# Kernel tuning notes

Measured on AMD Instinct MI355X. Metric: run time of the kernel, lower is better.

## Reference

```python
import jax, jax.numpy as jnp
import numpy as np

B, L, H_IN, N_FLOWS = 65536, 256, 300, 4


def householder(v, z):
    # z_new = z - 2 * v * (v . z) / ||v||^2   (fused; same math as vvT bmm chain)
    vz = jnp.sum(v * z, axis=1, keepdims=True)      # [B,1]
    norm_sq = jnp.sum(v * v, axis=1, keepdims=True)  # [B,1]
    return z - 2.0 * v * (vz / norm_sq)


def setup_inputs() -> dict:
    key = jax.random.key(0)
    ks = jax.random.split(key, 6)
    z = jax.random.normal(ks[0], (B, L), dtype=jnp.float32)
    h = jax.random.normal(ks[1], (B, H_IN), dtype=jnp.float32)
    W0 = jax.random.normal(ks[2], (L, H_IN), dtype=jnp.float32) * 0.05
    b0 = jax.random.normal(ks[3], (L,), dtype=jnp.float32) * 0.05
    Ws = jax.random.normal(ks[4], (N_FLOWS - 1, L, L), dtype=jnp.float32) * 0.05
    bs = jax.random.normal(ks[5], (N_FLOWS - 1, L), dtype=jnp.float32) * 0.05
    return {"z": z, "h": h, "W0": W0, "b0": b0, "Ws": Ws, "bs": bs}


def reference(z, h, W0, b0, Ws, bs):
    v = h @ W0.T + b0            # Linear(300 -> L)
    z = householder(v, z)
    for i in range(Ws.shape[0]):  # small fixed chain (n_flows-1)
        v = v @ Ws[i].T + bs[i]   # Linear(L -> L)
        z = householder(v, z)
    return z
```

## Files before the change

kernel.cpp:

```cpp
#include <hip/hip_runtime.h>

typedef __attribute__((ext_vector_type(4))) float f32x4;
typedef __attribute__((ext_vector_type(8))) short bf16x8;
typedef __attribute__((ext_vector_type(2))) unsigned int u32x2;
typedef __attribute__((ext_vector_type(4))) unsigned int u32x4;
typedef unsigned short ushort_t;

#define B_ROWS 65536
#define L_DIM  256
#define H_IN_D 300
#define H_PAD  320
#define BM     64
#define LDW    328
#define NTH    256

__device__ __forceinline__ ushort_t f2bf(float f) {
  unsigned u = __builtin_bit_cast(unsigned, f);
  unsigned r = u + 0x7fffu + ((u >> 16) & 1u);
  return (ushort_t)(r >> 16);
}
__device__ __forceinline__ unsigned pk2(float lo, float hi) {
  return (unsigned)f2bf(lo) | ((unsigned)f2bf(hi) << 16);
}
__device__ __forceinline__ float bflo(unsigned u) { return __builtin_bit_cast(float, u << 16); }
__device__ __forceinline__ float bfhi(unsigned u) { return __builtin_bit_cast(float, u & 0xffff0000u); }

__global__ void cvt_w(const float* __restrict__ W0, const float* __restrict__ Ws,
                      ushort_t* __restrict__ W0b, ushort_t* __restrict__ Wsb) {
  int i = blockIdx.x * blockDim.x + threadIdx.x;
  int stride = gridDim.x * blockDim.x;
  for (int t = i; t < 256 * H_PAD; t += stride) {
    int n = t / H_PAD, k = t - n * H_PAD;
    W0b[t] = (k < H_IN_D) ? f2bf(W0[n * H_IN_D + k]) : (ushort_t)0;
  }
  for (int t = i; t < 3 * 256 * 256; t += stride) Wsb[t] = f2bf(Ws[t]);
}

template<int KSTEPS>
__device__ __forceinline__ void gemm_acc(
    const ushort_t* __restrict__ Slds,
    const ushort_t* __restrict__ Wg, int ldb,
    int wave, int r, int g, f32x4 (&acc)[4][4])
{
  const ushort_t* xb = Wg + (wave * 64 + r) * ldb + g * 8;
  const ushort_t* yb = Slds + r * LDW + g * 8;
#pragma unroll
  for (int ks = 0; ks < KSTEPS; ++ks) {
    bf16x8 x[4];
#pragma unroll
    for (int nt = 0; nt < 4; ++nt) x[nt] = *(const bf16x8*)(xb + nt * 16 * ldb + ks * 32);
    bf16x8 y[4];
#pragma unroll
    for (int mt = 0; mt < 4; ++mt) y[mt] = *(const bf16x8*)(yb + mt * 16 * LDW + ks * 32);
#pragma unroll
    for (int nt = 0; nt < 4; ++nt) {
      acc[nt][0] = __builtin_amdgcn_mfma_f32_16x16x32_bf16(x[nt], y[0], acc[nt][0], 0, 0, 0);
      acc[nt][1] = __builtin_amdgcn_mfma_f32_16x16x32_bf16(x[nt], y[1], acc[nt][1], 0, 0, 0);
      acc[nt][2] = __builtin_amdgcn_mfma_f32_16x16x32_bf16(x[nt], y[2], acc[nt][2], 0, 0, 0);
      acc[nt][3] = __builtin_amdgcn_mfma_f32_16x16x32_bf16(x[nt], y[3], acc[nt][3], 0, 0, 0);
    }
  }
}

__device__ __forceinline__ void epi_write(
    f32x4 (&acc)[4][4], const float* __restrict__ bias,
    ushort_t* __restrict__ Slds, int wave, int r, int g)
{
#pragma unroll
  for (int nt = 0; nt < 4; ++nt) {
    const int n0 = wave * 64 + nt * 16 + g * 4;
    f32x4 bv = *(const f32x4*)(bias + n0);
#pragma unroll
    for (int mt = 0; mt < 4; ++mt) {
      float v0 = acc[nt][mt][0] + bv[0];
      float v1 = acc[nt][mt][1] + bv[1];
      float v2 = acc[nt][mt][2] + bv[2];
      float v3 = acc[nt][mt][3] + bv[3];
      u32x2 p; p[0] = pk2(v0, v1); p[1] = pk2(v2, v3);
      *(u32x2*)&Slds[(mt * 16 + r) * LDW + n0] = p;
    }
  }
}

__device__ __forceinline__ void dot_update(const ushort_t* __restrict__ V,
                                           int wave, int r, int g, float (&zr)[64])
{
  const ushort_t* vp = V + (wave * 16 + r) * LDW + g * 64;
  float vz = 0.f, vv = 0.f;
#pragma unroll
  for (int jb = 0; jb < 8; ++jb) {
    u32x4 q = *(const u32x4*)(vp + jb * 8);
#pragma unroll
    for (int w = 0; w < 4; ++w) {
      unsigned u = q[w];
      float f0 = bflo(u), f1 = bfhi(u);
      int i = jb * 8 + w * 2;
      vz = fmaf(f0, zr[i], vz);     vv = fmaf(f0, f0, vv);
      vz = fmaf(f1, zr[i + 1], vz); vv = fmaf(f1, f1, vv);
    }
  }
  vz += __shfl_xor(vz, 16); vv += __shfl_xor(vv, 16);
  vz += __shfl_xor(vz, 32); vv += __shfl_xor(vv, 32);
  float a = 2.f * vz / vv;
#pragma unroll
  for (int jb = 0; jb < 8; ++jb) {
    u32x4 q = *(const u32x4*)(vp + jb * 8);
#pragma unroll
    for (int w = 0; w < 4; ++w) {
      unsigned u = q[w];
      int i = jb * 8 + w * 2;
      zr[i]     = fmaf(-a, bflo(u), zr[i]);
      zr[i + 1] = fmaf(-a, bfhi(u), zr[i + 1]);
    }
  }
}

__global__ __launch_bounds__(NTH, 2) void flow_fused(
    const float* __restrict__ z, const float* __restrict__ h,
    const ushort_t* __restrict__ W0b, const float* __restrict__ b0,
    const ushort_t* __restrict__ Wsb, const float* __restrict__ bs,
    float* __restrict__ out)
{
  __shared__ __align__(16) ushort_t S[BM * LDW];

  const int tid  = threadIdx.x;
  const int wave = tid >> 6;
  const int lane = tid & 63;
  const int r    = lane & 15;
  const int g    = lane >> 4;
  const int row0 = blockIdx.x * BM;

  for (int row = wave; row < BM; row += 4) {
    const float* hrow = h + (row0 + row) * H_IN_D;
    f32x4 m4 = *(const f32x4*)(hrow + 4 * lane);
    u32x2 pm; pm[0] = pk2(m4[0], m4[1]); pm[1] = pk2(m4[2], m4[3]);
    *(u32x2*)&S[row * LDW + 4 * lane] = pm;
    if (lane < 16) {
      f32x4 t4 = {0.f, 0.f, 0.f, 0.f};
      if (lane < 11) t4 = *(const f32x4*)(hrow + 256 + 4 * lane);
      u32x2 pt; pt[0] = pk2(t4[0], t4[1]); pt[1] = pk2(t4[2], t4[3]);
      *(u32x2*)&S[row * LDW + 256 + 4 * lane] = pt;
    }
  }

  float zr[64];
  const int zrow = wave * 16 + r;
  {
    const float* zp = z + (row0 + zrow) * L_DIM + g * 64;
#pragma unroll
    for (int j = 0; j < 16; ++j) {
      f32x4 v = *(const f32x4*)(zp + j * 4);
      zr[j * 4 + 0] = v[0]; zr[j * 4 + 1] = v[1];
      zr[j * 4 + 2] = v[2]; zr[j * 4 + 3] = v[3];
    }
  }

  __syncthreads();

  {
    f32x4 acc[4][4];
#pragma unroll
    for (int a = 0; a < 4; ++a)
#pragma unroll
      for (int b = 0; b < 4; ++b) { acc[a][b][0]=0.f; acc[a][b][1]=0.f; acc[a][b][2]=0.f; acc[a][b][3]=0.f; }
    gemm_acc<10>(S, W0b, H_PAD, wave, r, g, acc);
    __syncthreads();
    epi_write(acc, b0, S, wave, r, g);
  }
  __syncthreads();
  dot_update(S, wave, r, g, zr);

#pragma unroll
  for (int s = 0; s < 3; ++s) {
    f32x4 acc[4][4];
#pragma unroll
    for (int a = 0; a < 4; ++a)
#pragma unroll
      for (int b = 0; b < 4; ++b) { acc[a][b][0]=0.f; acc[a][b][1]=0.f; acc[a][b][2]=0.f; acc[a][b][3]=0.f; }
    gemm_acc<8>(S, Wsb + s * 256 * 256, 256, wave, r, g, acc);
    __syncthreads();
    epi_write(acc, bs + s * 256, S, wave, r, g);
    __syncthreads();
    dot_update(S, wave, r, g, zr);
  }

  {
    float* op = out + (row0 + zrow) * L_DIM + g * 64;
#pragma unroll
    for (int j = 0; j < 16; ++j) {
      f32x4 v;
      v[0] = zr[j * 4 + 0]; v[1] = zr[j * 4 + 1];
      v[2] = zr[j * 4 + 2]; v[3] = zr[j * 4 + 3];
      *(f32x4*)(op + j * 4) = v;
    }
  }
}

extern "C" void kernel_launch(void* const* d_in, const int* in_sizes, int n_in,
                              void* d_out, int out_size, void* d_ws, size_t ws_size,
                              hipStream_t stream) {
  const float* z  = (const float*)d_in[0];
  const float* h  = (const float*)d_in[1];
  const float* W0 = (const float*)d_in[2];
  const float* b0 = (const float*)d_in[3];
  const float* Ws = (const float*)d_in[4];
  const float* bs = (const float*)d_in[5];
  float* out = (float*)d_out;

  ushort_t* W0b = (ushort_t*)d_ws;
  ushort_t* Wsb = W0b + 256 * H_PAD;

  hipLaunchKernelGGL(cvt_w, dim3(256), dim3(NTH), 0, stream, W0, Ws, W0b, Wsb);
  hipLaunchKernelGGL(flow_fused, dim3(B_ROWS / BM), dim3(NTH), 0, stream,
                     z, h, W0b, b0, Wsb, bs, out);
}
```

Baseline: 134.7 us.

## Precompose linear chain into per-stage matrices applied directly to h

Because each v is an affine function of h, the weights are composed on device (M_i = W_i·M_{i-1}, c_i = W_i c_{i-1} + b_i) by small prep kernels, and the main kernel computes every v from h with independent K=320 GEMMs. This removes the serial dependence on bf16-rounded v and drops the LDS write-back of v between stages. The Householder dot products are now done on the MFMA accumulators in registers, with a cross-wave reduction through shared memory. In exchange the per-row GEMM work rises (K=320 instead of 256 for three stages), three extra serial prep launches are added, and composing the products may change rounding behavior.

```diff
diff --git a/kernel.cpp b/kernel.cpp
--- a/kernel.cpp
+++ b/kernel.cpp
@@ -3,15 +3,13 @@
 typedef __attribute__((ext_vector_type(4))) float f32x4;
 typedef __attribute__((ext_vector_type(8))) short bf16x8;
 typedef __attribute__((ext_vector_type(2))) unsigned int u32x2;
-typedef __attribute__((ext_vector_type(4))) unsigned int u32x4;
 typedef unsigned short ushort_t;
 
-#define B_ROWS 65536
 #define L_DIM  256
 #define H_IN_D 300
-#define H_PAD  320
+#define KP     320
 #define BM     64
-#define LDW    328
+#define LDH    328
 #define NTH    256
 
 __device__ __forceinline__ ushort_t f2bf(float f) {
@@ -22,106 +20,62 @@
 __device__ __forceinline__ unsigned pk2(float lo, float hi) {
   return (unsigned)f2bf(lo) | ((unsigned)f2bf(hi) << 16);
 }
-__device__ __forceinline__ float bflo(unsigned u) { return __builtin_bit_cast(float, u << 16); }
-__device__ __forceinline__ float bfhi(unsigned u) { return __builtin_bit_cast(float, u & 0xffff0000u); }
-
-__global__ void cvt_w(const float* __restrict__ W0, const float* __restrict__ Ws,
-                      ushort_t* __restrict__ W0b, ushort_t* __restrict__ Wsb) {
+
+__global__ void cvt0(const float* __restrict__ W0, ushort_t* __restrict__ Mb0) {
   int i = blockIdx.x * blockDim.x + threadIdx.x;
-  int stride = gridDim.x * blockDim.x;
-  for (int t = i; t < 256 * H_PAD; t += stride) {
-    int n = t / H_PAD, k = t - n * H_PAD;
-    W0b[t] = (k < H_IN_D) ? f2bf(W0[n * H_IN_D + k]) : (ushort_t)0;
+  if (i >= 256 * KP) return;
+  int n = i / KP, k = i - n * KP;
+  Mb0[i] = (k < H_IN_D) ? f2bf(W0[n * H_IN_D + k]) : (ushort_t)0;
+}
+
+__global__ __launch_bounds__(256) void comp(
+    const float* __restrict__ Wmat,
+    const float* __restrict__ Min,
+    const float* __restrict__ bvec,
+    const float* __restrict__ cin,
+    float* __restrict__ Mout,
+    float* __restrict__ cout,
+    ushort_t* __restrict__ Mb)
+{
+  __shared__ float wrow[256];
+  __shared__ float cbuf[256];
+  __shared__ float red[4];
+  const int n = blockIdx.x;
+  const int tid = threadIdx.x;
+  wrow[tid] = Wmat[n * 256 + tid];
+  cbuf[tid] = cin[tid];
+  __syncthreads();
+
+  float cp = wrow[tid] * cbuf[tid];
+  cp += __shfl_xor(cp, 1);  cp += __shfl_xor(cp, 2);  cp += __shfl_xor(cp, 4);
+  cp += __shfl_xor(cp, 8);  cp += __shfl_xor(cp, 16); cp += __shfl_xor(cp, 32);
+  if ((tid & 63) == 0) red[tid >> 6] = cp;
+
+  float a0 = 0.f, a1 = 0.f;
+  const int k1 = 256 + tid;
+#pragma unroll 8
+  for (int j = 0; j < 256; ++j) {
+    float w = wrow[j];
+    a0 = fmaf(w, Min[j * H_IN_D + tid], a0);
+    if (tid < 44) a1 = fmaf(w, Min[j * H_IN_D + k1], a1);
   }
-  for (int t = i; t < 3 * 256 * 256; t += stride) Wsb[t] = f2bf(Ws[t]);
-}
-
-template<int KSTEPS>
-__device__ __forceinline__ void gemm_acc(
-    const ushort_t* __restrict__ Slds,
-    const ushort_t* __restrict__ Wg, int ldb,
-    int wave, int r, int g, f32x4 (&acc)[4][4])
-{
-  const ushort_t* xb = Wg + (wave * 64 + r) * ldb + g * 8;
-  const ushort_t* yb = Slds + r * LDW + g * 8;
-#pragma unroll
-  for (int ks = 0; ks < KSTEPS; ++ks) {
-    bf16x8 x[4];
-#pragma unroll
-    for (int nt = 0; nt < 4; ++nt) x[nt] = *(const bf16x8*)(xb + nt * 16 * ldb + ks * 32);
-    bf16x8 y[4];
-#pragma unroll
-    for (int mt = 0; mt < 4; ++mt) y[mt] = *(const bf16x8*)(yb + mt * 16 * LDW + ks * 32);
-#pragma unroll
-    for (int nt = 0; nt < 4; ++nt) {
-      acc[nt][0] = __builtin_amdgcn_mfma_f32_16x16x32_bf16(x[nt], y[0], acc[nt][0], 0, 0, 0);
-      acc[nt][1] = __builtin_amdgcn_mfma_f32_16x16x32_bf16(x[nt], y[1], acc[nt][1], 0, 0, 0);
-      acc[nt][2] = __builtin_amdgcn_mfma_f32_16x16x32_bf16(x[nt], y[2], acc[nt][2], 0, 0, 0);
-      acc[nt][3] = __builtin_amdgcn_mfma_f32_16x16x32_bf16(x[nt], y[3], acc[nt][3], 0, 0, 0);
-    }
-  }
-}
-
-__device__ __forceinline__ void epi_write(
-    f32x4 (&acc)[4][4], const float* __restrict__ bias,
-    ushort_t* __restrict__ Slds, int wave, int r, int g)
-{
-#pragma unroll
-  for (int nt = 0; nt < 4; ++nt) {
-    const int n0 = wave * 64 + nt * 16 + g * 4;
-    f32x4 bv = *(const f32x4*)(bias + n0);
-#pragma unroll
-    for (int mt = 0; mt < 4; ++mt) {
-      float v0 = acc[nt][mt][0] + bv[0];
-      float v1 = acc[nt][mt][1] + bv[1];
-      float v2 = acc[nt][mt][2] + bv[2];
-      float v3 = acc[nt][mt][3] + bv[3];
-      u32x2 p; p[0] = pk2(v0, v1); p[1] = pk2(v2, v3);
-      *(u32x2*)&Slds[(mt * 16 + r) * LDW + n0] = p;
-    }
-  }
-}
-
-__device__ __forceinline__ void dot_update(const ushort_t* __restrict__ V,
-                                           int wave, int r, int g, float (&zr)[64])
-{
-  const ushort_t* vp = V + (wave * 16 + r) * LDW + g * 64;
-  float vz = 0.f, vv = 0.f;
-#pragma unroll
-  for (int jb = 0; jb < 8; ++jb) {
-    u32x4 q = *(const u32x4*)(vp + jb * 8);
-#pragma unroll
-    for (int w = 0; w < 4; ++w) {
-      unsigned u = q[w];
-      float f0 = bflo(u), f1 = bfhi(u);
-      int i = jb * 8 + w * 2;
-      vz = fmaf(f0, zr[i], vz);     vv = fmaf(f0, f0, vv);
-      vz = fmaf(f1, zr[i + 1], vz); vv = fmaf(f1, f1, vv);
-    }
-  }
-  vz += __shfl_xor(vz, 16); vv += __shfl_xor(vv, 16);
-  vz += __shfl_xor(vz, 32); vv += __shfl_xor(vv, 32);
-  float a = 2.f * vz / vv;
-#pragma unroll
-  for (int jb = 0; jb < 8; ++jb) {
-    u32x4 q = *(const u32x4*)(vp + jb * 8);
-#pragma unroll
-    for (int w = 0; w < 4; ++w) {
-      unsigned u = q[w];
-      int i = jb * 8 + w * 2;
-      zr[i]     = fmaf(-a, bflo(u), zr[i]);
-      zr[i + 1] = fmaf(-a, bfhi(u), zr[i + 1]);
-    }
-  }
+  __syncthreads();
+  if (tid == 0) cout[n] = red[0] + red[1] + red[2] + red[3] + bvec[n];
+
+  Mout[n * H_IN_D + tid] = a0;
+  Mb[n * KP + tid] = f2bf(a0);
+  if (tid < 44) { Mout[n * H_IN_D + k1] = a1; Mb[n * KP + k1] = f2bf(a1); }
+  if (tid >= 236) Mb[n * KP + (tid + 64)] = (ushort_t)0;
 }
 
 __global__ __launch_bounds__(NTH, 2) void flow_fused(
     const float* __restrict__ z, const float* __restrict__ h,
-    const ushort_t* __restrict__ W0b, const float* __restrict__ b0,
-    const ushort_t* __restrict__ Wsb, const float* __restrict__ bs,
-    float* __restrict__ out)
+    const ushort_t* __restrict__ Mb, const float* __restrict__ b0,
+    const float* __restrict__ cvecs, float* __restrict__ out)
 {
-  __shared__ __align__(16) ushort_t S[BM * LDW];
+  __shared__ __align__(16) ushort_t hl[BM * LDH];
+  __shared__ float pvz[2][4][64];
+  __shared__ float pvv[2][4][64];
 
   const int tid  = threadIdx.x;
   const int wave = tid >> 6;
@@ -129,71 +83,111 @@
   const int r    = lane & 15;
   const int g    = lane >> 4;
   const int row0 = blockIdx.x * BM;
+  const int c0   = wave * 64;
 
   for (int row = wave; row < BM; row += 4) {
     const float* hrow = h + (row0 + row) * H_IN_D;
     f32x4 m4 = *(const f32x4*)(hrow + 4 * lane);
     u32x2 pm; pm[0] = pk2(m4[0], m4[1]); pm[1] = pk2(m4[2], m4[3]);
-    *(u32x2*)&S[row * LDW + 4 * lane] = pm;
+    *(u32x2*)&hl[row * LDH + 4 * lane] = pm;
     if (lane < 16) {
       f32x4 t4 = {0.f, 0.f, 0.f, 0.f};
       if (lane < 11) t4 = *(const f32x4*)(hrow + 256 + 4 * lane);
       u32x2 pt; pt[0] = pk2(t4[0], t4[1]); pt[1] = pk2(t4[2], t4[3]);
-      *(u32x2*)&S[row * LDW + 256 + 4 * lane] = pt;
+      *(u32x2*)&hl[row * LDH + 256 + 4 * lane] = pt;
     }
   }
 
-  float zr[64];
-  const int zrow = wave * 16 + r;
-  {
-    const float* zp = z + (row0 + zrow) * L_DIM + g * 64;
-#pragma unroll
-    for (int j = 0; j < 16; ++j) {
-      f32x4 v = *(const f32x4*)(zp + j * 4);
-      zr[j * 4 + 0] = v[0]; zr[j * 4 + 1] = v[1];
-      zr[j * 4 + 2] = v[2]; zr[j * 4 + 3] = v[3];
+  f32x4 zr[4][4];
+#pragma unroll
+  for (int mt = 0; mt < 4; ++mt)
+#pragma unroll
+    for (int nt = 0; nt < 4; ++nt)
+      zr[mt][nt] = *(const f32x4*)(z + (row0 + mt * 16 + r) * L_DIM + c0 + nt * 16 + g * 4);
+
+  __syncthreads();
+
+  const ushort_t* yb = hl + r * LDH + g * 8;
+
+#pragma unroll
+  for (int s = 0; s < 4; ++s) {
+    const ushort_t* W   = Mb + s * (256 * KP);
+    const float*   bias = (s == 0) ? b0 : (cvecs + (s - 1) * 256);
+    const int pb = s & 1;
+
+    f32x4 acc[4][4];
+#pragma unroll
+    for (int a = 0; a < 4; ++a)
+#pragma unroll
+      for (int b = 0; b < 4; ++b) { acc[a][b][0]=0.f; acc[a][b][1]=0.f; acc[a][b][2]=0.f; acc[a][b][3]=0.f; }
+
+    const ushort_t* xb = W + (c0 + r) * KP + g * 8;
+#pragma unroll
+    for (int ks = 0; ks < 10; ++ks) {
+      bf16x8 x[4];
+#pragma unroll
+      for (int nt = 0; nt < 4; ++nt) x[nt] = *(const bf16x8*)(xb + nt * 16 * KP + ks * 32);
+      bf16x8 y[4];
+#pragma unroll
+      for (int mt = 0; mt < 4; ++mt) y[mt] = *(const bf16x8*)(yb + mt * 16 * LDH + ks * 32);
+#pragma unroll
+      for (int nt = 0; nt < 4; ++nt) {
+        acc[nt][0] = __builtin_amdgcn_mfma_f32_16x16x32_bf16(x[nt], y[0], acc[nt][0], 0, 0, 0);
+        acc[nt][1] = __builtin_amdgcn_mfma_f32_16x16x32_bf16(x[nt], y[1], acc[nt][1], 0, 0, 0);
+        acc[nt][2] = __builtin_amdgcn_mfma_f32_16x16x32_bf16(x[nt], y[2], acc[nt][2], 0, 0, 0);
+        acc[nt][3] = __builtin_amdgcn_mfma_f32_16x16x32_bf16(x[nt], y[3], acc[nt][3], 0, 0, 0);
+      }
+    }
+
+    float vz[4] = {0.f, 0.f, 0.f, 0.f};
+    float vv[4] = {0.f, 0.f, 0.f, 0.f};
+#pragma unroll
+    for (int nt = 0; nt < 4; ++nt) {
+      f32x4 bv = *(const f32x4*)(bias + c0 + nt * 16 + g * 4);
+#pragma unroll
+      for (int mt = 0; mt < 4; ++mt) {
+#pragma unroll
+        for (int j = 0; j < 4; ++j) {
+          float v = acc[nt][mt][j] + bv[j];
+          acc[nt][mt][j] = v;
+          vz[mt] = fmaf(v, zr[mt][nt][j], vz[mt]);
+          vv[mt] = fmaf(v, v, vv[mt]);
+        }
+      }
+    }
+#pragma unroll
+    for (int mt = 0; mt < 4; ++mt) {
+      vz[mt] += __shfl_xor(vz[mt], 16); vz[mt] += __shfl_xor(vz[mt], 32);
+      vv[mt] += __shfl_xor(vv[mt], 16); vv[mt] += __shfl_xor(vv[mt], 32);
+    }
+    if (lane < 16) {
+#pragma unroll
+      for (int mt = 0; mt < 4; ++mt) {
+        pvz[pb][wave][mt * 16 + r] = vz[mt];
+        pvv[pb][wave][mt * 16 + r] = vv[mt];
+      }
+    }
+    __syncthreads();
+
+#pragma unroll
+    for (int mt = 0; mt < 4; ++mt) {
+      const int rw = mt * 16 + r;
+      float sz = pvz[pb][0][rw] + pvz[pb][1][rw] + pvz[pb][2][rw] + pvz[pb][3][rw];
+      float sv = pvv[pb][0][rw] + pvv[pb][1][rw] + pvv[pb][2][rw] + pvv[pb][3][rw];
+      float a = 2.f * sz / sv;
+#pragma unroll
+      for (int nt = 0; nt < 4; ++nt)
+#pragma unroll
+        for (int j = 0; j < 4; ++j)
+          zr[mt][nt][j] = fmaf(-a, acc[nt][mt][j], zr[mt][nt][j]);
     }
   }
 
-  __syncthreads();
-
-  {
-    f32x4 acc[4][4];
-#pragma unroll
-    for (int a = 0; a < 4; ++a)
-#pragma unroll
-      for (int b = 0; b < 4; ++b) { acc[a][b][0]=0.f; acc[a][b][1]=0.f; acc[a][b][2]=0.f; acc[a][b][3]=0.f; }
-    gemm_acc<10>(S, W0b, H_PAD, wave, r, g, acc);
-    __syncthreads();
-    epi_write(acc, b0, S, wave, r, g);
-  }
-  __syncthreads();
-  dot_update(S, wave, r, g, zr);
-
-#pragma unroll
-  for (int s = 0; s < 3; ++s) {
-    f32x4 acc[4][4];
-#pragma unroll
-    for (int a = 0; a < 4; ++a)
-#pragma unroll
-      for (int b = 0; b < 4; ++b) { acc[a][b][0]=0.f; acc[a][b][1]=0.f; acc[a][b][2]=0.f; acc[a][b][3]=0.f; }
-    gemm_acc<8>(S, Wsb + s * 256 * 256, 256, wave, r, g, acc);
-    __syncthreads();
-    epi_write(acc, bs + s * 256, S, wave, r, g);
-    __syncthreads();
-    dot_update(S, wave, r, g, zr);
-  }
-
-  {
-    float* op = out + (row0 + zrow) * L_DIM + g * 64;
-#pragma unroll
-    for (int j = 0; j < 16; ++j) {
-      f32x4 v;
-      v[0] = zr[j * 4 + 0]; v[1] = zr[j * 4 + 1];
-      v[2] = zr[j * 4 + 2]; v[3] = zr[j * 4 + 3];
-      *(f32x4*)(op + j * 4) = v;
-    }
-  }
+#pragma unroll
+  for (int mt = 0; mt < 4; ++mt)
+#pragma unroll
+    for (int nt = 0; nt < 4; ++nt)
+      *(f32x4*)(out + (row0 + mt * 16 + r) * L_DIM + c0 + nt * 16 + g * 4) = zr[mt][nt];
 }
 
 extern "C" void kernel_launch(void* const* d_in, const int* in_sizes, int n_in,
@@ -207,10 +201,19 @@
   const float* bs = (const float*)d_in[5];
   float* out = (float*)d_out;
 
-  ushort_t* W0b = (ushort_t*)d_ws;
-  ushort_t* Wsb = W0b + 256 * H_PAD;
-
-  hipLaunchKernelGGL(cvt_w, dim3(256), dim3(NTH), 0, stream, W0, Ws, W0b, Wsb);
-  hipLaunchKernelGGL(flow_fused, dim3(B_ROWS / BM), dim3(NTH), 0, stream,
-                     z, h, W0b, b0, Wsb, bs, out);
-}
+  ushort_t* Mb  = (ushort_t*)d_ws;
+  float*    Mc1 = (float*)((char*)d_ws + 655360);
+  float*    Mc2 = (float*)((char*)d_ws + 962560);
+  float*    Mc3 = (float*)((char*)d_ws + 1269760);
+  float*    cv  = (float*)((char*)d_ws + 1576960);
+
+  hipLaunchKernelGGL(cvt0, dim3((256 * KP + 255) / 256), dim3(256), 0, stream, W0, Mb);
+  hipLaunchKernelGGL(comp, dim3(256), dim3(256), 0, stream,
+                     Ws,             W0,  bs,       b0,       Mc1, cv,       Mb + 1 * 256 * KP);
+  hipLaunchKernelGGL(comp, dim3(256), dim3(256), 0, stream,
+                     Ws + 65536,     Mc1, bs + 256, cv,       Mc2, cv + 256, Mb + 2 * 256 * KP);
+  hipLaunchKernelGGL(comp, dim3(256), dim3(256), 0, stream,
+                     Ws + 131072,    Mc2, bs + 512, cv + 256, Mc3, cv + 512, Mb + 3 * 256 * KP);
+  hipLaunchKernelGGL(flow_fused, dim3(65536 / BM), dim3(NTH), 0, stream,
+                     z, h, Mb, b0, cv, out);
+}
```

After: 378.2 us. +180.8%, slower.
